# Optimization experiments

Hardware: AMD Instinct MI355X
Metric: run time of the kernel (lower is better)

The kernel has to match this reference:

```python
import jax, jax.numpy as jnp
import numpy as np

D_MODEL = 1024
N_HEADS = 16
D_K = D_MODEL // N_HEADS
THETA = 10000.0
BATCH, SEQ = 2, 2048


def setup_inputs() -> dict:
    key = jax.random.key(0)
    k1, k2, k3 = jax.random.split(key, 3)
    std_qkv = float(np.sqrt(2.0 / (3 * D_MODEL + D_MODEL)))
    std_o = float(np.sqrt(2.0 / (D_MODEL + D_MODEL)))
    return {
        "x": jax.random.normal(k1, (BATCH, SEQ, D_MODEL), dtype=jnp.float32),
        "w_qkv": jax.random.normal(k2, (3 * D_MODEL, D_MODEL), dtype=jnp.float32) * std_qkv,
        "w_o": jax.random.normal(k3, (D_MODEL, D_MODEL), dtype=jnp.float32) * std_o,
        "token_positions": jnp.arange(SEQ, dtype=jnp.int32),
    }


def _rope(x, token_positions):
    # x: [..., s, d_k]; interleaved rotary embedding
    d_k = x.shape[-1]
    freqs = jnp.arange(0, d_k, 2, dtype=jnp.float32) / d_k          # [d_k/2]
    inv_freqs = 1.0 / (THETA ** freqs)
    angles = token_positions.astype(jnp.float32)[:, None] * inv_freqs  # [s, d_k/2]
    cos, sin = jnp.cos(angles), jnp.sin(angles)
    x_even, x_odd = x[..., 0::2], x[..., 1::2]
    rot_even = x_even * cos - x_odd * sin
    rot_odd = x_even * sin + x_odd * cos
    # interleave back: out[..., 2i] = rot_even[i], out[..., 2i+1] = rot_odd[i]
    return jnp.stack([rot_even, rot_odd], axis=-1).reshape(x.shape)


def reference(x, w_qkv, w_o, token_positions):
    b, s, _ = x.shape
    qkv = jnp.einsum('oi,bsi->bso', w_qkv, x)                        # [b, s, 3*d_model]
    q, k, v = jnp.split(qkv, 3, axis=-1)
    def to_heads(t):
        return t.reshape(b, s, N_HEADS, D_K).transpose(0, 2, 1, 3)  # [b, h, s, d]
    q, k, v = to_heads(q), to_heads(k), to_heads(v)
    q = _rope(q, token_positions)
    k = _rope(k, token_positions)
    scores = jnp.einsum('bhqd,bhkd->bhqk', q, k) / jnp.sqrt(jnp.float32(D_K))
    causal = jnp.tril(jnp.ones((s, s), dtype=bool))
    scores = jnp.where(causal, scores, -jnp.inf)
    attn = jax.nn.softmax(scores, axis=-1)
    y = jnp.einsum('bhqk,bhkd->bhqd', attn, v)
    y = y.transpose(0, 2, 1, 3).reshape(b, s, D_MODEL)
    return jnp.einsum('oi,bsi->bso', w_o, y)
```

## Files before the change

kernel.cpp:

```cpp
#include <hip/hip_runtime.h>
#include <math.h>

#define DEV __device__ __forceinline__

typedef __attribute__((ext_vector_type(8))) short bf16x8;
typedef __attribute__((ext_vector_type(4))) float f32x4;
typedef __attribute__((ext_vector_type(4))) unsigned int u32x4;

typedef __attribute__((address_space(3))) unsigned int lds_u32;
typedef const __attribute__((address_space(1))) unsigned int glb_u32;

DEV void gload16(const unsigned short* g, unsigned short* l) {
  __builtin_amdgcn_global_load_lds((glb_u32*)g, (lds_u32*)l, 16, 0, 0);
}

DEV bf16x8 lds_read8(const unsigned short* base, unsigned int byteoff) {
  return *reinterpret_cast<const bf16x8*>(
      reinterpret_cast<const char*>(base) + byteoff);
}

DEV float fexp2(float x) { return __builtin_amdgcn_exp2f(x); }

DEV unsigned short f2bf(float f) {
  union { float f; unsigned int u; } v; v.f = f;
  unsigned int u = v.u;
  unsigned int r = (u + 0x7fffu + ((u >> 16) & 1u)) >> 16;
  return (unsigned short)r;
}
DEV float bf2f(unsigned short h) {
  union { unsigned int u; float f; } v; v.u = ((unsigned int)h) << 16;
  return v.f;
}
DEV unsigned int cvtpk_bf16(float lo, float hi) {
  unsigned int r;
  asm("v_cvt_pk_bf16_f32 %0, %1, %2" : "=v"(r) : "v"(lo), "v"(hi));
  return r;
}

__global__ void cvt3_f32_bf16(const float* __restrict__ ina,
                              unsigned short* __restrict__ outa, int n4a,
                              const float* __restrict__ inb,
                              unsigned short* __restrict__ outb, int n4b,
                              const float* __restrict__ inc,
                              unsigned short* __restrict__ outc, int n4c) {
  int stride = gridDim.x * blockDim.x;
  int total = n4a + n4b + n4c;
  for (int i = blockIdx.x * blockDim.x + threadIdx.x; i < total; i += stride) {
    const float* src;
    unsigned short* dst;
    int j = i;
    if (j < n4a) {
      src = ina; dst = outa;
    } else if ((j -= n4a) < n4b) {
      src = inb; dst = outb;
    } else {
      j -= n4b; src = inc; dst = outc;
    }
    float4 f = reinterpret_cast<const float4*>(src)[j];
    ushort4 o;
    o.x = f2bf(f.x); o.y = f2bf(f.y); o.z = f2bf(f.z); o.w = f2bf(f.w);
    reinterpret_cast<ushort4*>(dst)[j] = o;
  }
}

__global__ __launch_bounds__(512, 2) void gemm8_qkv(const unsigned short* __restrict__ A,
                                                    const unsigned short* __restrict__ B,
                                                    unsigned short* __restrict__ C) {
  constexpr int K = 1024;
  constexpr int NK = 16;
  __shared__ unsigned short Ls[2][32768];

  const int tid = threadIdx.x;
  const int lane = tid & 63, wid = tid >> 6;
  const int wm = (wid >> 2) * 128;
  const int wn = (wid & 3) * 64;
  const int fr = lane & 15, kq = lane >> 4;

  int bid = blockIdx.x;
  int swz = (bid & 7) * 24 + (bid >> 3);
  int tm = swz & 15, tn = swz >> 4;
  const int arow0 = tm * 256, brow0 = tn * 256;

  const int subrow = lane >> 3;
  const int scol = ((lane & 7) ^ subrow) * 8;
  const unsigned short* aSrc = A + (size_t)(arow0 + wid * 8 + subrow) * K + scol;
  const unsigned short* bSrc = B + (size_t)(brow0 + wid * 8 + subrow) * K + scol;

  unsigned aoff[2], boff[2];
#pragma unroll
  for (int ks = 0; ks < 2; ks++) {
    unsigned x = ((unsigned)((ks * 4 + kq) ^ (fr & 7))) * 16;
    aoff[ks] = (unsigned)((wm + fr) * 128) + x;
    boff[ks] = 32768u + (unsigned)((wn + fr) * 128) + x;
  }

  f32x4 acc[8][4] = {};

#define STAGE_A8(BUF, H, T)                                                  \
  {                                                                          \
    gload16(aSrc + (size_t)((H) * 128) * K + (T) * 64,                       \
            &Ls[BUF][((H) * 128 + wid * 8) * 64]);                           \
    gload16(aSrc + (size_t)((H) * 128 + 64) * K + (T) * 64,                  \
            &Ls[BUF][((H) * 128 + 64 + wid * 8) * 64]);                      \
  }
#define STAGE_B8(BUF, H, T)                                                  \
  {                                                                          \
    gload16(bSrc + (size_t)((H) * 128) * K + (T) * 64,                       \
            &Ls[BUF][16384 + ((H) * 128 + wid * 8) * 64]);                   \
    gload16(bSrc + (size_t)((H) * 128 + 64) * K + (T) * 64,                  \
            &Ls[BUF][16384 + ((H) * 128 + 64 + wid * 8) * 64]);              \
  }

  STAGE_A8(0, 0, 0) STAGE_A8(0, 1, 0)
  STAGE_B8(0, 0, 0) STAGE_B8(0, 1, 0)
  STAGE_B8(1, 0, 1) STAGE_B8(1, 1, 1)
  asm volatile("s_waitcnt vmcnt(4)" ::: "memory");
  __builtin_amdgcn_s_barrier();

#define PHASE8(BUF, P, DO_STAGE)                                              \
  {                                                                           \
    bf16x8 af[2][2];                                                          \
    _Pragma("unroll") for (int mm = 0; mm < 2; mm++)                          \
      _Pragma("unroll") for (int ks = 0; ks < 2; ks++)                        \
        af[mm][ks] = lds_read8(Ls[BUF], aoff[ks] + ((P) * 2 + mm) * 2048);    \
    DO_STAGE                                                                  \
    __builtin_amdgcn_s_setprio(1);                                            \
    _Pragma("unroll") for (int mm = 0; mm < 2; mm++)                          \
      _Pragma("unroll") for (int j = 0; j < 4; j++)                           \
        _Pragma("unroll") for (int ks = 0; ks < 2; ks++)                      \
          acc[(P) * 2 + mm][j] = __builtin_amdgcn_mfma_f32_16x16x32_bf16(     \
              af[mm][ks], bq[j][ks], acc[(P) * 2 + mm][j], 0, 0, 0);          \
    __builtin_amdgcn_s_setprio(0);                                            \
  }

#define TILE8(T, BUF)                                                          \
  {                                                                            \
    bf16x8 bq[4][2];                                                           \
    _Pragma("unroll") for (int j = 0; j < 4; j++)                              \
      _Pragma("unroll") for (int ks = 0; ks < 2; ks++)                         \
        bq[j][ks] = lds_read8(Ls[BUF], boff[ks] + j * 2048);                   \
    PHASE8(BUF, 0, {                                                           \
      if ((T) + 1 < NK) { STAGE_A8(BUF ^ 1, 0, (T) + 1) STAGE_A8(BUF ^ 1, 1, (T) + 1) } \
    })                                                                         \
    __builtin_amdgcn_s_barrier();                                              \
    PHASE8(BUF, 1, { if ((T) + 2 < NK) STAGE_B8(BUF, 0, (T) + 2) })            \
    __builtin_amdgcn_s_barrier();                                              \
    PHASE8(BUF, 2, { if ((T) + 2 < NK) STAGE_B8(BUF, 1, (T) + 2) })            \
    __builtin_amdgcn_s_barrier();                                              \
    PHASE8(BUF, 3, {})                                                         \
    if ((T) + 2 < NK) {                                                        \
      asm volatile("s_waitcnt vmcnt(4)" ::: "memory");                         \
    } else {                                                                   \
      asm volatile("s_waitcnt vmcnt(0)" ::: "memory");                         \
    }                                                                          \
    __builtin_amdgcn_s_barrier();                                              \
    __builtin_amdgcn_sched_barrier(0);                                         \
  }

#pragma unroll 1
  for (int t = 0; t < NK; t += 2) {
    TILE8(t, 0)
    TILE8(t + 1, 1)
  }
#undef TILE8
#undef PHASE8
#undef STAGE_A8
#undef STAGE_B8

#pragma unroll
  for (int m = 0; m < 8; m++) {
#pragma unroll
    for (int j = 0; j < 4; j++) {
      size_t row = (size_t)(arow0 + wm + m * 16 + kq * 4);
      size_t col = (size_t)(brow0 + wn + j * 16 + fr);
#pragma unroll
      for (int r = 0; r < 4; r++)
        C[(row + r) * 3072 + col] = f2bf(acc[m][j][r]);
    }
  }
}

template <bool BF16_OUT>
__global__ __launch_bounds__(256) void gemm_bt(const unsigned short* __restrict__ A,
                                               const unsigned short* __restrict__ B,
                                               void* __restrict__ Cv,
                                               int M, int N, int K) {
  __shared__ unsigned short Ab[2][4096];
  __shared__ unsigned short Bb[2][4096];
  const int tid = threadIdx.x;
  const int lane = tid & 63, wid = tid >> 6;
  const int wm = (wid >> 1) * 64, wn = (wid & 1) * 64;
  const int fr = lane & 15, kq = lane >> 4;
  const int arow0 = blockIdx.x * 128;
  const int brow0 = blockIdx.y * 128;
  const int srow = wid * 16 + (lane >> 2);
  const int sslot = (((lane & 3) ^ ((lane >> 2) & 3))) * 8;
  const unsigned short* aptr = A + (size_t)(arow0 + srow) * K + sslot;
  const unsigned short* bptr = B + (size_t)(brow0 + srow) * K + sslot;
  unsigned int offa[4], offb[4];
#pragma unroll
  for (int i = 0; i < 4; i++) {
    offa[i] = (unsigned)((wm + i * 16 + fr) * 64 + ((kq ^ (fr & 3)) * 16));
    offb[i] = (unsigned)((wn + i * 16 + fr) * 64 + ((kq ^ (fr & 3)) * 16));
  }
  f32x4 acc[4][4] = {};

#define GSTAGE(BI)                                                 \
  {                                                                \
    gload16(aptr, &Ab[BI][wid * 512]);                             \
    gload16(aptr + (size_t)64 * K, &Ab[BI][2048 + wid * 512]);     \
    gload16(bptr, &Bb[BI][wid * 512]);                             \
    gload16(bptr + (size_t)64 * K, &Bb[BI][2048 + wid * 512]);     \
    aptr += 32;                                                    \
    bptr += 32;                                                    \
  }

#define GCOMP(BI)                                                                      \
  {                                                                                    \
    bf16x8 af[4], bfr[4];                                                              \
    _Pragma("unroll") for (int i = 0; i < 4; i++) af[i] = lds_read8(Ab[BI], offa[i]);  \
    _Pragma("unroll") for (int j = 0; j < 4; j++) bfr[j] = lds_read8(Bb[BI], offb[j]); \
    _Pragma("unroll") for (int i = 0; i < 4; i++)                                      \
      _Pragma("unroll") for (int j = 0; j < 4; j++)                                    \
        acc[i][j] = __builtin_amdgcn_mfma_f32_16x16x32_bf16(af[i], bfr[j], acc[i][j], 0, 0, 0); \
  }

  const int nk = K >> 5;
  GSTAGE(0);
  for (int ks = 0; ks < nk; ks += 2) {
    asm volatile("s_waitcnt lgkmcnt(0)" ::: "memory");
    __builtin_amdgcn_s_barrier();
    GSTAGE(1);
    asm volatile("s_waitcnt vmcnt(4)" ::: "memory");
    GCOMP(0);
    asm volatile("s_waitcnt lgkmcnt(0)" ::: "memory");
    __builtin_amdgcn_s_barrier();
    if (ks + 2 < nk) {
      GSTAGE(0);
      asm volatile("s_waitcnt vmcnt(4)" ::: "memory");
    } else {
      asm volatile("s_waitcnt vmcnt(0)" ::: "memory");
    }
    GCOMP(1);
  }
#undef GSTAGE
#undef GCOMP

#pragma unroll
  for (int i = 0; i < 4; i++) {
#pragma unroll
    for (int j = 0; j < 4; j++) {
#pragma unroll
      for (int r = 0; r < 4; r++) {
        size_t row = (size_t)(arow0 + wm + i * 16 + kq * 4 + r);
        size_t col = (size_t)(brow0 + wn + j * 16 + fr);
        if (BF16_OUT)
          ((unsigned short*)Cv)[row * N + col] = f2bf(acc[i][j][r]);
        else
          ((float*)Cv)[row * N + col] = acc[i][j][r];
      }
    }
  }
}

__global__ __launch_bounds__(256) void rope_vtrans_kernel(unsigned short* __restrict__ qkv,
                                                          const int* __restrict__ pos,
                                                          unsigned short* __restrict__ vt) {
  int bid0 = blockIdx.x;
  int t = threadIdx.x;
  if (bid0 < 4096) {
    int m = bid0;
    int s = m & 2047;
    __shared__ float Cl[32], Sl[32];
    if (t < 32) {
      float position = (float)pos[s];
      float inv = __expf(-(float)t * (9.210340371976184f / 32.0f));
      float ang = position * inv;
      Cl[t] = cosf(ang);
      Sl[t] = sinf(ang);
    }
    __syncthreads();
    const float QS = 0.18033688011112042f;
    int h = t >> 4, g = t & 15;
    float c0 = Cl[2 * g], s0 = Sl[2 * g], c1 = Cl[2 * g + 1], s1 = Sl[2 * g + 1];
    size_t base = (size_t)m * 3072 + h * 64 + 4 * g;
    ushort4 qv = *reinterpret_cast<ushort4*>(&qkv[base]);
    float qe0 = bf2f(qv.x), qo0 = bf2f(qv.y), qe1 = bf2f(qv.z), qo1 = bf2f(qv.w);
    qv.x = f2bf((qe0 * c0 - qo0 * s0) * QS);
    qv.y = f2bf((qe0 * s0 + qo0 * c0) * QS);
    qv.z = f2bf((qe1 * c1 - qo1 * s1) * QS);
    qv.w = f2bf((qe1 * s1 + qo1 * c1) * QS);
    *reinterpret_cast<ushort4*>(&qkv[base]) = qv;
    size_t kb = base + 1024;
    ushort4 kv = *reinterpret_cast<ushort4*>(&qkv[kb]);
    float ke0 = bf2f(kv.x), ko0 = bf2f(kv.y), ke1 = bf2f(kv.z), ko1 = bf2f(kv.w);
    kv.x = f2bf(ke0 * c0 - ko0 * s0);
    kv.y = f2bf(ke0 * s0 + ko0 * c0);
    kv.z = f2bf(ke1 * c1 - ko1 * s1);
    kv.w = f2bf(ke1 * s1 + ko1 * c1);
    *reinterpret_cast<ushort4*>(&qkv[kb]) = kv;
  } else {
    int bid = bid0 - 4096;
    int sb = bid & 31;
    int bh = bid >> 5;
    int h = bh & 15, b = bh >> 4;
    __shared__ unsigned short tile[64][72];
    int sl = t >> 2, c0 = (t & 3) * 16;
    const unsigned short* src = qkv + (size_t)(b * 2048 + sb * 64) * 3072 + 2048 + h * 64;
    *reinterpret_cast<bf16x8*>(&tile[sl][c0]) =
        *reinterpret_cast<const bf16x8*>(&src[(size_t)sl * 3072 + c0]);
    *reinterpret_cast<bf16x8*>(&tile[sl][c0 + 8]) =
        *reinterpret_cast<const bf16x8*>(&src[(size_t)sl * 3072 + c0 + 8]);
    __syncthreads();
    int d = t >> 2, p0 = (t & 3) * 16;
    unsigned short* dst = vt + ((size_t)bh * 64 + d) * 2048 + sb * 64 + p0;
    bf16x8 o0, o1;
#pragma unroll
    for (int i = 0; i < 8; i++) {
      int p = p0 + i;
      int s_in = (p & 32) + ((p >> 2) & 1) * 16 + ((p >> 3) & 3) * 4 + (p & 3);
      o0[i] = (short)tile[s_in][d];
    }
#pragma unroll
    for (int i = 0; i < 8; i++) {
      int p = p0 + 8 + i;
      int s_in = (p & 32) + ((p >> 2) & 1) * 16 + ((p >> 3) & 3) * 4 + (p & 3);
      o1[i] = (short)tile[s_in][d];
    }
    *reinterpret_cast<bf16x8*>(dst) = o0;
    *reinterpret_cast<bf16x8*>(dst + 8) = o1;
  }
}

__global__ __launch_bounds__(256, 4) void attn_kernel(const unsigned short* __restrict__ qkv,
                                                      const unsigned short* __restrict__ vt,
                                                      unsigned short* __restrict__ Y) {
  int bid = blockIdx.x;
  int g = bid & 255;
  int r = bid >> 8;
  int bh = g & 31;
  int t0 = g >> 3 & 0;
  t0 = g >> 5;
  int qt = (r == 0) ? t0 : (r == 1) ? (15 - t0) : (r == 2) ? (16 + t0) : (31 - t0);
  int h = bh & 15, b = bh >> 4;
  int tid = threadIdx.x, lane = tid & 63, wid = tid >> 6;
  int fr = lane & 15, kq = lane >> 4;
  int qbase = qt * 64 + wid * 16;

  const size_t mrow0 = (size_t)b * 2048;
  const unsigned short* Qp = qkv + (mrow0 + qbase) * 3072 + h * 64;
  const unsigned short* Kp = qkv + mrow0 * 3072 + 1024 + h * 64;
  const unsigned short* Vp = vt + ((size_t)bh * 64) * 2048;

  __shared__ unsigned short Klds[2][5120];
  __shared__ unsigned short Vlds[2][5120];

  bf16x8 qf[2];
#pragma unroll
  for (int ks = 0; ks < 2; ks++)
    qf[ks] = *reinterpret_cast<const bf16x8*>(&Qp[(size_t)fr * 3072 + ks * 32 + kq * 8]);

  const int srow = tid >> 3;
  const int schunk = (tid & 7) ^ (srow & 7);
  const unsigned short* kstage = Kp + (size_t)srow * 3072 + schunk * 8;
  const unsigned short* vstage = Vp + (size_t)srow * 2048 + schunk * 8;

  unsigned int offk[8], offv[8];
#pragma unroll
  for (int gg = 0; gg < 4; gg++)
#pragma unroll
    for (int ks = 0; ks < 2; ks++) {
      int R = gg * 16 + fr;
      offk[gg * 2 + ks] = (unsigned)(R * 128 + (((4 * ks + kq) ^ (R & 7)) * 16));
    }
#pragma unroll
  for (int db = 0; db < 4; db++)
#pragma unroll
    for (int hf = 0; hf < 2; hf++) {
      int d = db * 16 + fr;
      offv[db * 2 + hf] = (unsigned)(d * 128 + (((4 * hf + kq) ^ (d & 7)) * 16));
    }

  bf16x8 vones;
#pragma unroll
  for (int i = 0; i < 8; i++) vones[i] = (short)0x3F80;

  f32x4 acc[4] = {};
  f32x4 lacc = {};
  const int q_lane = qbase + fr;
  const int ntiles = qt + 1;

#define STAGE(BI)                                                     \
  {                                                                   \
    gload16(kstage, &Klds[BI][wid * 512]);                            \
    gload16(kstage + (size_t)32 * 3072, &Klds[BI][2048 + wid * 512]); \
    gload16(vstage, &Vlds[BI][wid * 512]);                            \
    gload16(vstage + 32 * 2048, &Vlds[BI][2048 + wid * 512]);         \
    kstage += (size_t)64 * 3072;                                      \
    vstage += 64;                                                     \
  }

#define TILE_COMPUTE(T, BI)                                                           \
  {                                                                                   \
    const bool masked_ = ((T) == qt);                                                 \
    f32x4 sc[4] = {};                                                                 \
    __builtin_amdgcn_s_setprio(1);                                                    \
    _Pragma("unroll") for (int gg = 0; gg < 4; gg++) {                                \
      _Pragma("unroll") for (int ks = 0; ks < 2; ks++) {                              \
        bf16x8 kf = lds_read8(Klds[BI], offk[gg * 2 + ks]);                           \
        sc[gg] = __builtin_amdgcn_mfma_f32_16x16x32_bf16(kf, qf[ks], sc[gg], 0, 0, 0);\
      }                                                                               \
    }                                                                                 \
    __builtin_amdgcn_s_setprio(0);                                                    \
    float p[16];                                                                      \
    _Pragma("unroll") for (int gg = 0; gg < 4; gg++)                                  \
      _Pragma("unroll") for (int rr = 0; rr < 4; rr++) {                              \
        float v = sc[gg][rr];                                                         \
        if (masked_) {                                                                \
          int k = (T) * 64 + gg * 16 + kq * 4 + rr;                                   \
          if (k > q_lane) v = -1e30f;                                                 \
        }                                                                             \
        p[gg * 4 + rr] = fexp2(v);                                                    \
      }                                                                               \
    u32x4 W0 = {cvtpk_bf16(p[0], p[1]), cvtpk_bf16(p[2], p[3]),                       \
                cvtpk_bf16(p[4], p[5]), cvtpk_bf16(p[6], p[7])};                      \
    u32x4 W1 = {cvtpk_bf16(p[8], p[9]), cvtpk_bf16(p[10], p[11]),                     \
                cvtpk_bf16(p[12], p[13]), cvtpk_bf16(p[14], p[15])};                  \
    bf16x8 pa0 = *reinterpret_cast<bf16x8*>(&W0);                                     \
    bf16x8 pa1 = *reinterpret_cast<bf16x8*>(&W1);                                     \
    __builtin_amdgcn_s_setprio(1);                                                    \
    _Pragma("unroll") for (int db = 0; db < 4; db++) {                                \
      bf16x8 vf0 = lds_read8(Vlds[BI], offv[db * 2]);                                 \
      acc[db] = __builtin_amdgcn_mfma_f32_16x16x32_bf16(vf0, pa0, acc[db], 0, 0, 0);  \
      bf16x8 vf1 = lds_read8(Vlds[BI], offv[db * 2 + 1]);                             \
      acc[db] = __builtin_amdgcn_mfma_f32_16x16x32_bf16(vf1, pa1, acc[db], 0, 0, 0);  \
    }                                                                                 \
    lacc = __builtin_amdgcn_mfma_f32_16x16x32_bf16(vones, pa0, lacc, 0, 0, 0);        \
    lacc = __builtin_amdgcn_mfma_f32_16x16x32_bf16(vones, pa1, lacc, 0, 0, 0);        \
    __builtin_amdgcn_s_setprio(0);                                                    \
  }

  STAGE(0);
  for (int t = 0; t < ntiles; t += 2) {
    asm volatile("s_waitcnt lgkmcnt(0)" ::: "memory");
    __builtin_amdgcn_s_barrier();
    if (t + 1 < ntiles) {
      STAGE(1);
      asm volatile("s_waitcnt vmcnt(4)" ::: "memory");
    } else {
      asm volatile("s_waitcnt vmcnt(0)" ::: "memory");
    }
    TILE_COMPUTE(t, 0);
    if (t + 1 >= ntiles) break;
    asm volatile("s_waitcnt lgkmcnt(0)" ::: "memory");
    __builtin_amdgcn_s_barrier();
    if (t + 2 < ntiles) {
      STAGE(0);
      asm volatile("s_waitcnt vmcnt(4)" ::: "memory");
    } else {
      asm volatile("s_waitcnt vmcnt(0)" ::: "memory");
    }
    TILE_COMPUTE(t + 1, 1);
  }
#undef TILE_COMPUTE
#undef STAGE

  float inv = 1.0f / lacc[0];
  unsigned short* yp = Y + (mrow0 + qbase + fr) * 1024 + h * 64 + kq * 4;
#pragma unroll
  for (int db = 0; db < 4; db++) {
    ushort4 o;
    o.x = f2bf(acc[db][0] * inv);
    o.y = f2bf(acc[db][1] * inv);
    o.z = f2bf(acc[db][2] * inv);
    o.w = f2bf(acc[db][3] * inv);
    *reinterpret_cast<ushort4*>(yp + db * 16) = o;
  }
}

extern "C" void kernel_launch(void* const* d_in, const int* in_sizes, int n_in,
                              void* d_out, int out_size, void* d_ws, size_t ws_size,
                              hipStream_t stream) {
  const float* x     = (const float*)d_in[0];
  const float* w_qkv = (const float*)d_in[1];
  const float* w_o   = (const float*)d_in[2];
  const int*   pos   = (const int*)d_in[3];
  float* out = (float*)d_out;

  unsigned char* ws = (unsigned char*)d_ws;
  unsigned short* x_bf    = (unsigned short*)(ws);
  unsigned short* wqkv_bf = (unsigned short*)(ws + 8388608);
  unsigned short* wo_bf   = (unsigned short*)(ws + 14680064);
  unsigned short* qkv     = (unsigned short*)(ws + 16777216);
  unsigned short* vt      = (unsigned short*)(ws + 41943040);
  unsigned short* y       = (unsigned short*)(ws + 50331648);

  cvt3_f32_bf16<<<1536, 256, 0, stream>>>(x, x_bf, 4096 * 1024 / 4,
                                          w_qkv, wqkv_bf, 3072 * 1024 / 4,
                                          w_o, wo_bf, 1024 * 1024 / 4);

  gemm8_qkv<<<192, 512, 0, stream>>>(x_bf, wqkv_bf, qkv);

  rope_vtrans_kernel<<<5120, 256, 0, stream>>>(qkv, pos, vt);

  attn_kernel<<<1024, 256, 0, stream>>>(qkv, vt, y);

  gemm_bt<false><<<dim3(32, 8), 256, 0, stream>>>(y, wo_bf, (void*)out, 4096, 1024, 1024);
}
```

Before: 113.5 us.

## Double query tile per attention block to reuse K/V tiles across two query groups

```diff
diff --git a/kernel.cpp b/kernel.cpp
--- a/kernel.cpp
+++ b/kernel.cpp
@@ -332,33 +332,35 @@
   }
 }
 
-__global__ __launch_bounds__(256, 4) void attn_kernel(const unsigned short* __restrict__ qkv,
+__global__ __launch_bounds__(256, 2) void attn_kernel(const unsigned short* __restrict__ qkv,
                                                       const unsigned short* __restrict__ vt,
                                                       unsigned short* __restrict__ Y) {
   int bid = blockIdx.x;
   int g = bid & 255;
   int r = bid >> 8;
   int bh = g & 31;
-  int t0 = g >> 3 & 0;
-  t0 = g >> 5;
-  int qt = (r == 0) ? t0 : (r == 1) ? (15 - t0) : (r == 2) ? (16 + t0) : (31 - t0);
+  int t0 = g >> 5;
+  int qt = r ? (15 - t0) : t0;
   int h = bh & 15, b = bh >> 4;
   int tid = threadIdx.x, lane = tid & 63, wid = tid >> 6;
   int fr = lane & 15, kq = lane >> 4;
-  int qbase = qt * 64 + wid * 16;
+  int qbase = qt * 128 + wid * 32;
 
   const size_t mrow0 = (size_t)b * 2048;
   const unsigned short* Qp = qkv + (mrow0 + qbase) * 3072 + h * 64;
   const unsigned short* Kp = qkv + mrow0 * 3072 + 1024 + h * 64;
   const unsigned short* Vp = vt + ((size_t)bh * 64) * 2048;
 
-  __shared__ unsigned short Klds[2][5120];
-  __shared__ unsigned short Vlds[2][5120];
-
-  bf16x8 qf[2];
-#pragma unroll
-  for (int ks = 0; ks < 2; ks++)
-    qf[ks] = *reinterpret_cast<const bf16x8*>(&Qp[(size_t)fr * 3072 + ks * 32 + kq * 8]);
+  __shared__ unsigned short Klds[2][8192];
+  __shared__ unsigned short Vlds[2][8192];
+
+  bf16x8 qf[2][2];
+#pragma unroll
+  for (int qg = 0; qg < 2; qg++)
+#pragma unroll
+    for (int ks = 0; ks < 2; ks++)
+      qf[qg][ks] = *reinterpret_cast<const bf16x8*>(
+          &Qp[(size_t)(qg * 16 + fr) * 3072 + ks * 32 + kq * 8]);
 
   const int srow = tid >> 3;
   const int schunk = (tid & 7) ^ (srow & 7);
@@ -385,10 +387,10 @@
 #pragma unroll
   for (int i = 0; i < 8; i++) vones[i] = (short)0x3F80;
 
-  f32x4 acc[4] = {};
-  f32x4 lacc = {};
-  const int q_lane = qbase + fr;
-  const int ntiles = qt + 1;
+  f32x4 acc[2][4] = {};
+  f32x4 lacc[2] = {};
+  const int Tm = qbase >> 6;
+  const int ntiles = 2 * qt + 2;
 
 #define STAGE(BI)                                                     \
   {                                                                   \
@@ -400,44 +402,52 @@
     vstage += 64;                                                     \
   }
 
-#define TILE_COMPUTE(T, BI)                                                           \
-  {                                                                                   \
-    const bool masked_ = ((T) == qt);                                                 \
-    f32x4 sc[4] = {};                                                                 \
-    __builtin_amdgcn_s_setprio(1);                                                    \
-    _Pragma("unroll") for (int gg = 0; gg < 4; gg++) {                                \
-      _Pragma("unroll") for (int ks = 0; ks < 2; ks++) {                              \
-        bf16x8 kf = lds_read8(Klds[BI], offk[gg * 2 + ks]);                           \
-        sc[gg] = __builtin_amdgcn_mfma_f32_16x16x32_bf16(kf, qf[ks], sc[gg], 0, 0, 0);\
-      }                                                                               \
-    }                                                                                 \
-    __builtin_amdgcn_s_setprio(0);                                                    \
-    float p[16];                                                                      \
-    _Pragma("unroll") for (int gg = 0; gg < 4; gg++)                                  \
-      _Pragma("unroll") for (int rr = 0; rr < 4; rr++) {                              \
-        float v = sc[gg][rr];                                                         \
-        if (masked_) {                                                                \
-          int k = (T) * 64 + gg * 16 + kq * 4 + rr;                                   \
-          if (k > q_lane) v = -1e30f;                                                 \
-        }                                                                             \
-        p[gg * 4 + rr] = fexp2(v);                                                    \
-      }                                                                               \
-    u32x4 W0 = {cvtpk_bf16(p[0], p[1]), cvtpk_bf16(p[2], p[3]),                       \
-                cvtpk_bf16(p[4], p[5]), cvtpk_bf16(p[6], p[7])};                      \
-    u32x4 W1 = {cvtpk_bf16(p[8], p[9]), cvtpk_bf16(p[10], p[11]),                     \
-                cvtpk_bf16(p[12], p[13]), cvtpk_bf16(p[14], p[15])};                  \
-    bf16x8 pa0 = *reinterpret_cast<bf16x8*>(&W0);                                     \
-    bf16x8 pa1 = *reinterpret_cast<bf16x8*>(&W1);                                     \
-    __builtin_amdgcn_s_setprio(1);                                                    \
-    _Pragma("unroll") for (int db = 0; db < 4; db++) {                                \
-      bf16x8 vf0 = lds_read8(Vlds[BI], offv[db * 2]);                                 \
-      acc[db] = __builtin_amdgcn_mfma_f32_16x16x32_bf16(vf0, pa0, acc[db], 0, 0, 0);  \
-      bf16x8 vf1 = lds_read8(Vlds[BI], offv[db * 2 + 1]);                             \
-      acc[db] = __builtin_amdgcn_mfma_f32_16x16x32_bf16(vf1, pa1, acc[db], 0, 0, 0);  \
-    }                                                                                 \
-    lacc = __builtin_amdgcn_mfma_f32_16x16x32_bf16(vones, pa0, lacc, 0, 0, 0);        \
-    lacc = __builtin_amdgcn_mfma_f32_16x16x32_bf16(vones, pa1, lacc, 0, 0, 0);        \
-    __builtin_amdgcn_s_setprio(0);                                                    \
+#define TILE_COMPUTE(T, BI)                                                             \
+  if ((T) <= Tm) {                                                                      \
+    const bool masked_ = ((T) == Tm);                                                   \
+    f32x4 sc[2][4] = {};                                                                \
+    __builtin_amdgcn_s_setprio(1);                                                      \
+    _Pragma("unroll") for (int gg = 0; gg < 4; gg++) {                                  \
+      _Pragma("unroll") for (int ks = 0; ks < 2; ks++) {                                \
+        bf16x8 kf = lds_read8(Klds[BI], offk[gg * 2 + ks]);                             \
+        sc[0][gg] = __builtin_amdgcn_mfma_f32_16x16x32_bf16(kf, qf[0][ks], sc[0][gg], 0, 0, 0); \
+        sc[1][gg] = __builtin_amdgcn_mfma_f32_16x16x32_bf16(kf, qf[1][ks], sc[1][gg], 0, 0, 0); \
+      }                                                                                 \
+    }                                                                                   \
+    __builtin_amdgcn_s_setprio(0);                                                      \
+    bf16x8 pa[2][2];                                                                    \
+    _Pragma("unroll") for (int qg = 0; qg < 2; qg++) {                                  \
+      const int q_lane = qbase + qg * 16 + fr;                                          \
+      float p[16];                                                                      \
+      _Pragma("unroll") for (int gg = 0; gg < 4; gg++)                                  \
+        _Pragma("unroll") for (int rr = 0; rr < 4; rr++) {                              \
+          float v = sc[qg][gg][rr];                                                     \
+          if (masked_) {                                                                \
+            int k = (T) * 64 + gg * 16 + kq * 4 + rr;                                   \
+            if (k > q_lane) v = -1e30f;                                                 \
+          }                                                                             \
+          p[gg * 4 + rr] = fexp2(v);                                                    \
+        }                                                                               \
+      u32x4 W0 = {cvtpk_bf16(p[0], p[1]), cvtpk_bf16(p[2], p[3]),                       \
+                  cvtpk_bf16(p[4], p[5]), cvtpk_bf16(p[6], p[7])};                      \
+      u32x4 W1 = {cvtpk_bf16(p[8], p[9]), cvtpk_bf16(p[10], p[11]),                     \
+                  cvtpk_bf16(p[12], p[13]), cvtpk_bf16(p[14], p[15])};                  \
+      pa[qg][0] = *reinterpret_cast<bf16x8*>(&W0);                                      \
+      pa[qg][1] = *reinterpret_cast<bf16x8*>(&W1);                                      \
+    }                                                                                   \
+    __builtin_amdgcn_s_setprio(1);                                                      \
+    _Pragma("unroll") for (int db = 0; db < 4; db++) {                                  \
+      _Pragma("unroll") for (int hf = 0; hf < 2; hf++) {                                \
+        bf16x8 vf = lds_read8(Vlds[BI], offv[db * 2 + hf]);                             \
+        acc[0][db] = __builtin_amdgcn_mfma_f32_16x16x32_bf16(vf, pa[0][hf], acc[0][db], 0, 0, 0); \
+        acc[1][db] = __builtin_amdgcn_mfma_f32_16x16x32_bf16(vf, pa[1][hf], acc[1][db], 0, 0, 0); \
+      }                                                                                 \
+    }                                                                                   \
+    _Pragma("unroll") for (int qg = 0; qg < 2; qg++) {                                  \
+      lacc[qg] = __builtin_amdgcn_mfma_f32_16x16x32_bf16(vones, pa[qg][0], lacc[qg], 0, 0, 0); \
+      lacc[qg] = __builtin_amdgcn_mfma_f32_16x16x32_bf16(vones, pa[qg][1], lacc[qg], 0, 0, 0); \
+    }                                                                                   \
+    __builtin_amdgcn_s_setprio(0);                                                      \
   }
 
   STAGE(0);
@@ -465,16 +475,19 @@
 #undef TILE_COMPUTE
 #undef STAGE
 
-  float inv = 1.0f / lacc[0];
-  unsigned short* yp = Y + (mrow0 + qbase + fr) * 1024 + h * 64 + kq * 4;
-#pragma unroll
-  for (int db = 0; db < 4; db++) {
-    ushort4 o;
-    o.x = f2bf(acc[db][0] * inv);
-    o.y = f2bf(acc[db][1] * inv);
-    o.z = f2bf(acc[db][2] * inv);
-    o.w = f2bf(acc[db][3] * inv);
-    *reinterpret_cast<ushort4*>(yp + db * 16) = o;
+#pragma unroll
+  for (int qg = 0; qg < 2; qg++) {
+    float inv = 1.0f / lacc[qg][0];
+    unsigned short* yp = Y + (mrow0 + qbase + qg * 16 + fr) * 1024 + h * 64 + kq * 4;
+#pragma unroll
+    for (int db = 0; db < 4; db++) {
+      ushort4 o;
+      o.x = f2bf(acc[qg][db][0] * inv);
+      o.y = f2bf(acc[qg][db][1] * inv);
+      o.z = f2bf(acc[qg][db][2] * inv);
+      o.w = f2bf(acc[qg][db][3] * inv);
+      *reinterpret_cast<ushort4*>(yp + db * 16) = o;
+    }
   }
 }
 
@@ -503,7 +516,7 @@
 
   rope_vtrans_kernel<<<5120, 256, 0, stream>>>(qkv, pos, vt);
 
-  attn_kernel<<<1024, 256, 0, stream>>>(qkv, vt, y);
+  attn_kernel<<<512, 256, 0, stream>>>(qkv, vt, y);
 
   gemm_bt<false><<<dim3(32, 8), 256, 0, stream>>>(y, wo_bf, (void*)out, 4096, 1024, 1024);
 }
```

Result: slower. 119.8 us (+5.5%).
